# Kernel tuning notes

Hardware: AMD Instinct MI355X
Metric: run time of the kernel (lower is better)

The kernel has to match this reference:

```python
import jax, jax.numpy as jnp
import numpy as np

N_LEVELS = 16
N_FEATS = 2
LOG2_T = 19
BASE_RES = 16.0
FINEST_RES = 512.0
BOX_MIN = jnp.array([-1.0, -1.0, -1.0], dtype=jnp.float32)
BOX_MAX = jnp.array([1.0, 1.0, 1.0], dtype=jnp.float32)
# corner offsets, i (x) slowest, k (z) fastest -> index = 4*i + 2*j + k, matching BOX_OFFSETS
OFFSETS = jnp.array([[i, j, k] for i in (0, 1) for j in (0, 1) for k in (0, 1)], dtype=jnp.int32)  # [8,3]
PRIMES = jnp.array([73856093, 19349663, 83492791], dtype=jnp.int32)
HASH_MASK = (1 << LOG2_T) - 1


def setup_inputs() -> dict:
    key = jax.random.key(0)
    k1, k2 = jax.random.split(key)
    B = 1_000_000
    # points inside the bounding box
    x = jax.random.uniform(k1, (B, 3), dtype=jnp.float32, minval=-1.0, maxval=1.0)
    # nn.init.uniform_(w, a=-1e-4, b=1e-4)
    embeddings = jax.random.uniform(k2, (N_LEVELS, 1 << LOG2_T, N_FEATS), dtype=jnp.float32,
                                    minval=-1e-4, maxval=1e-4)
    return {"x": x, "embeddings": embeddings}


def _hash_encode(x, embeddings):
    # x: [B,3], embeddings: [L,T,F]
    b = jnp.exp((jnp.log(FINEST_RES) - jnp.log(BASE_RES)) / (N_LEVELS - 1))
    resolutions = jnp.floor(BASE_RES * b ** jnp.arange(N_LEVELS, dtype=jnp.float32))  # [L]
    xc = jnp.clip(x, BOX_MIN, BOX_MAX)

    def level_fn(table, res):
        grid_size = (BOX_MAX - BOX_MIN) / res  # [3]
        bl = jnp.floor((xc - BOX_MIN) / grid_size).astype(jnp.int32)  # [B,3]
        vmin = bl.astype(xc.dtype) * grid_size + BOX_MIN               # [B,3]
        w = (xc - vmin) / grid_size                                    # [B,3] in [0,1]
        idx = bl[:, None, :] + OFFSETS[None, :, :]                     # [B,8,3]
        prod = idx * PRIMES                                            # int32 wraparound, as in torch
        h = (prod[..., 0] ^ prod[..., 1] ^ prod[..., 2]) & HASH_MASK   # [B,8] in [0,2^19)
        emb = table[h]                                                 # [B,8,F] gather
        # trilinear weights: prod_d (o_d*w_d + (1-o_d)*(1-w_d))
        cw = jnp.prod(jnp.where(OFFSETS[None].astype(bool), w[:, None, :], 1.0 - w[:, None, :]), axis=-1)  # [B,8]
        return jnp.sum(cw[..., None] * emb, axis=1)                    # [B,F]

    outs = jax.vmap(level_fn)(embeddings, resolutions)                 # [L,B,F]
    B = x.shape[0]
    return jnp.transpose(outs, (1, 0, 2)).reshape(B, N_LEVELS * N_FEATS)


def reference(x, embeddings):
    return _hash_encode(x, embeddings)
```

## Files before the change

### kernel.cpp

```cpp
#include <hip/hip_runtime.h>
#include <stdint.h>

#define TMASK ((1u << 19) - 1u)
#define EMB_SCALE     8192.0f
#define EMB_INV_SCALE (1.0f / 8192.0f)

typedef float    vf2 __attribute__((ext_vector_type(2)));
typedef float    vf4 __attribute__((ext_vector_type(4)));
typedef _Float16 vh2 __attribute__((ext_vector_type(2)));
typedef _Float16 vh4 __attribute__((ext_vector_type(4)));

static __device__ const float GS_F[16] = {
    2.0f/16.0f, 2.0f/20.0f, 2.0f/25.0f, 2.0f/32.0f,
    2.0f/40.0f, 2.0f/50.0f, 2.0f/64.0f, 2.0f/80.0f,
    2.0f/101.0f, 2.0f/128.0f, 2.0f/161.0f, 2.0f/203.0f,
    2.0f/256.0f, 2.0f/322.0f, 2.0f/406.0f, 2.0f/512.0f};
static __device__ const float INVGS_F[16] = {
    8.0f, 10.0f, 12.5f, 16.0f,
    20.0f, 25.0f, 32.0f, 40.0f,
    50.5f, 64.0f, 80.5f, 101.5f,
    128.0f, 161.0f, 203.0f, 256.0f};

struct Corner8 { vf2 e[8]; float w[8]; };

__device__ __forceinline__ vf2 load_entry(const vf2* __restrict__ tb, uint32_t h) {
    return tb[h];
}
__device__ __forceinline__ vf2 load_entry(const vh2* __restrict__ tb, uint32_t h) {
    const vh2 v = tb[h];
    vf2 r; r.x = (float)v.x; r.y = (float)v.y;
    return r;
}

template <typename T>
__device__ __forceinline__ void gather_level(
    const T* __restrict__ tb, float cx, float cy, float cz,
    float gs, float ivg, Corner8& g)
{
    const float ux = (cx + 1.0f) * ivg;
    const float uy = (cy + 1.0f) * ivg;
    const float uz = (cz + 1.0f) * ivg;
    const float fx = floorf(ux), fy = floorf(uy), fz = floorf(uz);
    const int ix = (int)fx, iy = (int)fy, iz = (int)fz;
    const float wx = (cx - (fx * gs - 1.0f)) * ivg;
    const float wy = (cy - (fy * gs - 1.0f)) * ivg;
    const float wz = (cz - (fz * gs - 1.0f)) * ivg;

    const uint32_t px0 = (uint32_t)ix * 73856093u, px1 = px0 + 73856093u;
    const uint32_t py0 = (uint32_t)iy * 19349663u, py1 = py0 + 19349663u;
    const uint32_t pz0 = (uint32_t)iz * 83492791u, pz1 = pz0 + 83492791u;

    g.e[0] = load_entry(tb, (px0 ^ py0 ^ pz0) & TMASK);
    g.e[1] = load_entry(tb, (px0 ^ py0 ^ pz1) & TMASK);
    g.e[2] = load_entry(tb, (px0 ^ py1 ^ pz0) & TMASK);
    g.e[3] = load_entry(tb, (px0 ^ py1 ^ pz1) & TMASK);
    g.e[4] = load_entry(tb, (px1 ^ py0 ^ pz0) & TMASK);
    g.e[5] = load_entry(tb, (px1 ^ py0 ^ pz1) & TMASK);
    g.e[6] = load_entry(tb, (px1 ^ py1 ^ pz0) & TMASK);
    g.e[7] = load_entry(tb, (px1 ^ py1 ^ pz1) & TMASK);

    const float wxm = 1.0f - wx, wym = 1.0f - wy, wzm = 1.0f - wz;
    const float c00 = wxm * wym, c01 = wxm * wy;
    const float c10 = wx  * wym, c11 = wx  * wy;
    g.w[0] = c00 * wzm; g.w[1] = c00 * wz;
    g.w[2] = c01 * wzm; g.w[3] = c01 * wz;
    g.w[4] = c10 * wzm; g.w[5] = c10 * wz;
    g.w[6] = c11 * wzm; g.w[7] = c11 * wz;
}

__device__ __forceinline__ vf2 blend(const Corner8& g) {
    vf2 r;
    r.x = g.w[0]*g.e[0].x + g.w[1]*g.e[1].x + g.w[2]*g.e[2].x + g.w[3]*g.e[3].x
        + g.w[4]*g.e[4].x + g.w[5]*g.e[5].x + g.w[6]*g.e[6].x + g.w[7]*g.e[7].x;
    r.y = g.w[0]*g.e[0].y + g.w[1]*g.e[1].y + g.w[2]*g.e[2].y + g.w[3]*g.e[3].y
        + g.w[4]*g.e[4].y + g.w[5]*g.e[5].y + g.w[6]*g.e[6].y + g.w[7]*g.e[7].y;
    return r;
}

__global__ __launch_bounds__(256) void convert_kernel(
    const vf4* __restrict__ emb, vh4* __restrict__ tb, int n4)
{
    const int i = blockIdx.x * blockDim.x + threadIdx.x;
    if (i >= n4) return;
    const vf4 v = __builtin_nontemporal_load(emb + i);
    vh4 o;
    o.x = (_Float16)(v.x * EMB_SCALE);
    o.y = (_Float16)(v.y * EMB_SCALE);
    o.z = (_Float16)(v.z * EMB_SCALE);
    o.w = (_Float16)(v.w * EMB_SCALE);
    tb[i] = o;
}

template <typename T, bool SCALED>
__global__ __launch_bounds__(256) void level_kernel(
    const float* __restrict__ x,
    const T* __restrict__ tbl,
    vf2* __restrict__ ws,
    int B, int half, int l0, int l1)
{
    const int p0 = blockIdx.x * blockDim.x + threadIdx.x;
    if (p0 >= half) return;
    const int p1 = p0 + half;
    const bool has1 = p1 < B;
    const int p1c = has1 ? p1 : p0;

    const float ax = __builtin_nontemporal_load(x + 3*p0 + 0);
    const float ay = __builtin_nontemporal_load(x + 3*p0 + 1);
    const float az = __builtin_nontemporal_load(x + 3*p0 + 2);
    const float bx = __builtin_nontemporal_load(x + 3*p1c + 0);
    const float by = __builtin_nontemporal_load(x + 3*p1c + 1);
    const float bz = __builtin_nontemporal_load(x + 3*p1c + 2);

    const float cax = fminf(fmaxf(ax, -1.0f), 1.0f);
    const float cay = fminf(fmaxf(ay, -1.0f), 1.0f);
    const float caz = fminf(fmaxf(az, -1.0f), 1.0f);
    const float cbx = fminf(fmaxf(bx, -1.0f), 1.0f);
    const float cby = fminf(fmaxf(by, -1.0f), 1.0f);
    const float cbz = fminf(fmaxf(bz, -1.0f), 1.0f);

#pragma unroll 1
    for (int l = l0; l <= l1; ++l) {
        const float gs  = GS_F[l];
        const float ivg = INVGS_F[l];
        const T* __restrict__ tb = tbl + ((size_t)l << 19);

        Corner8 ga, gb;
        gather_level(tb, cax, cay, caz, gs, ivg, ga);
        gather_level(tb, cbx, cby, cbz, gs, ivg, gb);

        vf2 ra = blend(ga);
        vf2 rb = blend(gb);
        if constexpr (SCALED) {
            ra.x *= EMB_INV_SCALE; ra.y *= EMB_INV_SCALE;
            rb.x *= EMB_INV_SCALE; rb.y *= EMB_INV_SCALE;
        }

        __builtin_nontemporal_store(ra, &ws[(long)l * B + p0]);
        if (has1) __builtin_nontemporal_store(rb, &ws[(long)l * B + p1]);
    }
}

__global__ __launch_bounds__(256) void transpose_kernel(
    const vf2* __restrict__ ws, vf4* __restrict__ out, int B)
{
    __shared__ vf2 tile[16][257];
    const int t = threadIdx.x;
    const int base = blockIdx.x * 256;

#pragma unroll
    for (int l = 0; l < 16; ++l) {
        const int b = base + t;
        if (b < B) tile[l][t] = __builtin_nontemporal_load(&ws[(long)l * B + b]);
    }
    __syncthreads();

#pragma unroll
    for (int k = 0; k < 8; ++k) {
        const int flat = k * 256 + t;
        const int p = flat >> 3;
        const int j = flat & 7;
        if (base + p < B) {
            const vf2 a = tile[2*j][p];
            const vf2 c = tile[2*j+1][p];
            vf4 v; v.x = a.x; v.y = a.y; v.z = c.x; v.w = c.y;
            __builtin_nontemporal_store(v, &out[(long)base * 8 + flat]);
        }
    }
}

__global__ __launch_bounds__(256) void level_scatter_kernel(
    const float* __restrict__ x,
    const float* __restrict__ emb,
    vf2* __restrict__ out,
    int B, int l0, int l1)
{
    const int b = blockIdx.x * blockDim.x + threadIdx.x;
    if (b >= B) return;
    const float cx = fminf(fmaxf(x[3*b+0], -1.0f), 1.0f);
    const float cy = fminf(fmaxf(x[3*b+1], -1.0f), 1.0f);
    const float cz = fminf(fmaxf(x[3*b+2], -1.0f), 1.0f);
#pragma unroll 1
    for (int l = l0; l <= l1; ++l) {
        const vf2* __restrict__ tb = ((const vf2*)emb) + ((size_t)l << 19);
        Corner8 g;
        gather_level(tb, cx, cy, cz, GS_F[l], INVGS_F[l], g);
        out[(long)b * 16 + l] = blend(g);
    }
}

extern "C" void kernel_launch(void* const* d_in, const int* in_sizes, int n_in,
                              void* d_out, int out_size, void* d_ws, size_t ws_size,
                              hipStream_t stream) {
    const float* x   = (const float*)d_in[0];
    const float* emb = (const float*)d_in[1];
    const int B = in_sizes[0] / 3;

    const size_t tbl_bytes = (size_t)16 * 524288 * sizeof(vh2);
    const size_t wsl_bytes = (size_t)B * 16 * sizeof(vf2);

    vh2* tb = nullptr;
    vf2* ws = nullptr;
    if (ws_size >= tbl_bytes + wsl_bytes) {
        tb = (vh2*)d_ws;
        ws = (vf2*)((char*)d_ws + tbl_bytes);
    } else if (ws_size >= wsl_bytes && (size_t)out_size >= tbl_bytes) {
        tb = (vh2*)d_out;
        ws = (vf2*)d_ws;
    }

    if (tb) {
        const int n4 = 16 * 524288 * 2 / 4;
        convert_kernel<<<(n4 + 255) / 256, 256, 0, stream>>>(
            (const vf4*)emb, (vh4*)tb, n4);

        const int half = (B + 1) / 2;
        const int grid = (half + 255) / 256;
        level_kernel<vh2, true><<<grid, 256, 0, stream>>>(x, tb, ws, B, half, 0, 4);
        for (int l = 5; l < 16; ++l)
            level_kernel<vh2, true><<<grid, 256, 0, stream>>>(x, tb, ws, B, half, l, l);
        transpose_kernel<<<(B + 255) / 256, 256, 0, stream>>>(ws, (vf4*)d_out, B);
    } else if (ws_size >= wsl_bytes) {
        vf2* wsd = (vf2*)d_ws;
        const int half = (B + 1) / 2;
        const int grid = (half + 255) / 256;
        level_kernel<vf2, false><<<grid, 256, 0, stream>>>(
            x, (const vf2*)emb, wsd, B, half, 0, 5);
        for (int l = 6; l < 16; ++l)
            level_kernel<vf2, false><<<grid, 256, 0, stream>>>(
                x, (const vf2*)emb, wsd, B, half, l, l);
        transpose_kernel<<<(B + 255) / 256, 256, 0, stream>>>(wsd, (vf4*)d_out, B);
    } else {
        const int grid = (B + 255) / 256;
        vf2* o = (vf2*)d_out;
        level_scatter_kernel<<<grid, 256, 0, stream>>>(x, emb, o, B, 0, 5);
        for (int l = 6; l < 16; ++l)
            level_scatter_kernel<<<grid, 256, 0, stream>>>(x, emb, o, B, l, l);
    }
}
```

Baseline: 775.0 us.

## Fuse per-level gather kernels and transpose into a single monolithic kernel

Replaces the per-level launch sequence and the separate transpose pass with one kernel that computes all 16 levels per point pair, keeps results in registers, and transposes through shared memory directly into the output. This removes the level-major workspace write and read-back and most kernel launches. In exchange, all level tables are accessed concurrently, so per-level L2 locality of the hash table is lost, and register pressure rises from holding 32 vf2 results per thread.

```diff
diff --git a/kernel.cpp b/kernel.cpp
--- a/kernel.cpp
+++ b/kernel.cpp
@@ -92,24 +92,25 @@
 }
 
 template <typename T, bool SCALED>
-__global__ __launch_bounds__(256) void level_kernel(
+__global__ __launch_bounds__(256) void monolith_kernel(
     const float* __restrict__ x,
     const T* __restrict__ tbl,
-    vf2* __restrict__ ws,
-    int B, int half, int l0, int l1)
+    vf4* __restrict__ out,
+    int B, int half)
 {
-    const int p0 = blockIdx.x * blockDim.x + threadIdx.x;
-    if (p0 >= half) return;
-    const int p1 = p0 + half;
-    const bool has1 = p1 < B;
-    const int p1c = has1 ? p1 : p0;
+    const int t = threadIdx.x;
+    const int base = blockIdx.x * 256;
+    const int p0r = base + t;
+    const int p0 = p0r < half ? p0r : half - 1;
+    const int p1r = p0 + half;
+    const int p1 = p1r < B ? p1r : B - 1;
 
     const float ax = __builtin_nontemporal_load(x + 3*p0 + 0);
     const float ay = __builtin_nontemporal_load(x + 3*p0 + 1);
     const float az = __builtin_nontemporal_load(x + 3*p0 + 2);
-    const float bx = __builtin_nontemporal_load(x + 3*p1c + 0);
-    const float by = __builtin_nontemporal_load(x + 3*p1c + 1);
-    const float bz = __builtin_nontemporal_load(x + 3*p1c + 2);
+    const float bx = __builtin_nontemporal_load(x + 3*p1 + 0);
+    const float by = __builtin_nontemporal_load(x + 3*p1 + 1);
+    const float bz = __builtin_nontemporal_load(x + 3*p1 + 2);
 
     const float cax = fminf(fmaxf(ax, -1.0f), 1.0f);
     const float cay = fminf(fmaxf(ay, -1.0f), 1.0f);
@@ -118,8 +119,9 @@
     const float cby = fminf(fmaxf(by, -1.0f), 1.0f);
     const float cbz = fminf(fmaxf(bz, -1.0f), 1.0f);
 
-#pragma unroll 1
-    for (int l = l0; l <= l1; ++l) {
+    vf2 oa[16], ob[16];
+#pragma unroll
+    for (int l = 0; l < 16; ++l) {
         const float gs  = GS_F[l];
         const float ivg = INVGS_F[l];
         const T* __restrict__ tb = tbl + ((size_t)l << 19);
@@ -134,57 +136,43 @@
             ra.x *= EMB_INV_SCALE; ra.y *= EMB_INV_SCALE;
             rb.x *= EMB_INV_SCALE; rb.y *= EMB_INV_SCALE;
         }
-
-        __builtin_nontemporal_store(ra, &ws[(long)l * B + p0]);
-        if (has1) __builtin_nontemporal_store(rb, &ws[(long)l * B + p1]);
-    }
-}
-
-__global__ __launch_bounds__(256) void transpose_kernel(
-    const vf2* __restrict__ ws, vf4* __restrict__ out, int B)
-{
+        oa[l] = ra; ob[l] = rb;
+    }
+
     __shared__ vf2 tile[16][257];
-    const int t = threadIdx.x;
-    const int base = blockIdx.x * 256;
-
-#pragma unroll
-    for (int l = 0; l < 16; ++l) {
-        const int b = base + t;
-        if (b < B) tile[l][t] = __builtin_nontemporal_load(&ws[(long)l * B + b]);
-    }
+
+#pragma unroll
+    for (int l = 0; l < 16; ++l) tile[l][t] = oa[l];
     __syncthreads();
-
 #pragma unroll
     for (int k = 0; k < 8; ++k) {
         const int flat = k * 256 + t;
         const int p = flat >> 3;
         const int j = flat & 7;
-        if (base + p < B) {
+        if (base + p < half) {
             const vf2 a = tile[2*j][p];
             const vf2 c = tile[2*j+1][p];
             vf4 v; v.x = a.x; v.y = a.y; v.z = c.x; v.w = c.y;
-            __builtin_nontemporal_store(v, &out[(long)base * 8 + flat]);
+            __builtin_nontemporal_store(v, &out[(long)(base + p) * 8 + j]);
         }
     }
-}
-
-__global__ __launch_bounds__(256) void level_scatter_kernel(
-    const float* __restrict__ x,
-    const float* __restrict__ emb,
-    vf2* __restrict__ out,
-    int B, int l0, int l1)
-{
-    const int b = blockIdx.x * blockDim.x + threadIdx.x;
-    if (b >= B) return;
-    const float cx = fminf(fmaxf(x[3*b+0], -1.0f), 1.0f);
-    const float cy = fminf(fmaxf(x[3*b+1], -1.0f), 1.0f);
-    const float cz = fminf(fmaxf(x[3*b+2], -1.0f), 1.0f);
-#pragma unroll 1
-    for (int l = l0; l <= l1; ++l) {
-        const vf2* __restrict__ tb = ((const vf2*)emb) + ((size_t)l << 19);
-        Corner8 g;
-        gather_level(tb, cx, cy, cz, GS_F[l], INVGS_F[l], g);
-        out[(long)b * 16 + l] = blend(g);
+    __syncthreads();
+
+#pragma unroll
+    for (int l = 0; l < 16; ++l) tile[l][t] = ob[l];
+    __syncthreads();
+#pragma unroll
+    for (int k = 0; k < 8; ++k) {
+        const int flat = k * 256 + t;
+        const int p = flat >> 3;
+        const int j = flat & 7;
+        const long pt = (long)base + half + p;
+        if (pt < B) {
+            const vf2 a = tile[2*j][p];
+            const vf2 c = tile[2*j+1][p];
+            vf4 v; v.x = a.x; v.y = a.y; v.z = c.x; v.w = c.y;
+            __builtin_nontemporal_store(v, &out[pt * 8 + j]);
+        }
     }
 }
 
@@ -195,45 +183,19 @@
     const float* emb = (const float*)d_in[1];
     const int B = in_sizes[0] / 3;
 
+    const int half = (B + 1) / 2;
+    const int grid = (half + 255) / 256;
     const size_t tbl_bytes = (size_t)16 * 524288 * sizeof(vh2);
-    const size_t wsl_bytes = (size_t)B * 16 * sizeof(vf2);
-
-    vh2* tb = nullptr;
-    vf2* ws = nullptr;
-    if (ws_size >= tbl_bytes + wsl_bytes) {
-        tb = (vh2*)d_ws;
-        ws = (vf2*)((char*)d_ws + tbl_bytes);
-    } else if (ws_size >= wsl_bytes && (size_t)out_size >= tbl_bytes) {
-        tb = (vh2*)d_out;
-        ws = (vf2*)d_ws;
-    }
-
-    if (tb) {
+
+    if (ws_size >= tbl_bytes) {
+        vh2* tb = (vh2*)d_ws;
         const int n4 = 16 * 524288 * 2 / 4;
         convert_kernel<<<(n4 + 255) / 256, 256, 0, stream>>>(
             (const vf4*)emb, (vh4*)tb, n4);
-
-        const int half = (B + 1) / 2;
-        const int grid = (half + 255) / 256;
-        level_kernel<vh2, true><<<grid, 256, 0, stream>>>(x, tb, ws, B, half, 0, 4);
-        for (int l = 5; l < 16; ++l)
-            level_kernel<vh2, true><<<grid, 256, 0, stream>>>(x, tb, ws, B, half, l, l);
-        transpose_kernel<<<(B + 255) / 256, 256, 0, stream>>>(ws, (vf4*)d_out, B);
-    } else if (ws_size >= wsl_bytes) {
-        vf2* wsd = (vf2*)d_ws;
-        const int half = (B + 1) / 2;
-        const int grid = (half + 255) / 256;
-        level_kernel<vf2, false><<<grid, 256, 0, stream>>>(
-            x, (const vf2*)emb, wsd, B, half, 0, 5);
-        for (int l = 6; l < 16; ++l)
-            level_kernel<vf2, false><<<grid, 256, 0, stream>>>(
-                x, (const vf2*)emb, wsd, B, half, l, l);
-        transpose_kernel<<<(B + 255) / 256, 256, 0, stream>>>(wsd, (vf4*)d_out, B);
+        monolith_kernel<vh2, true><<<grid, 256, 0, stream>>>(
+            x, tb, (vf4*)d_out, B, half);
     } else {
-        const int grid = (B + 255) / 256;
-        vf2* o = (vf2*)d_out;
-        level_scatter_kernel<<<grid, 256, 0, stream>>>(x, emb, o, B, 0, 5);
-        for (int l = 6; l < 16; ++l)
-            level_scatter_kernel<<<grid, 256, 0, stream>>>(x, emb, o, B, l, l);
-    }
-}
+        monolith_kernel<vf2, false><<<grid, 256, 0, stream>>>(
+            x, (const vf2*)emb, (vf4*)d_out, B, half);
+    }
+}
```

New measurement: 884.9 us. 1.14x slower.
